# Kernel tuning notes

Hardware: AMD Instinct MI355X
Metric: run time of the kernel (lower is better)

## Reference

```python
import jax, jax.numpy as jnp
import numpy as np

NPOINT = 1024
NSAMPLE = 32
RADIUS = 0.2


def index_points2(points, idx):
    # points: (B,N,D), idx: (B,S) -> (B,S,D)
    return jnp.take_along_axis(points, idx[..., None], axis=1)


def index_points3(points, idx):
    # points: (B,N,D), idx: (B,S,K) -> (B,S,K,D)
    B, S, K = idx.shape
    flat = jnp.take_along_axis(points, idx.reshape(B, S * K)[..., None], axis=1)
    return flat.reshape(B, S, K, points.shape[-1])


def farthest_point_sampling(xyz, npoint):
    # xyz: (B,N,3) -> (B,npoint) int32 indices. First point deterministic (index 0).
    B, N, _ = xyz.shape
    first = jnp.zeros((B,), jnp.int32)
    chosen = jnp.zeros((B, npoint), jnp.int32).at[:, 0].set(first)
    first_xyz = index_points2(xyz, first[:, None])[:, 0, :]
    dist_min = jnp.sum((xyz - first_xyz[:, None, :]) ** 2, axis=-1)  # (B,N)

    def body(i, carry):
        chosen, dist_min = carry
        far = jnp.argmax(dist_min, axis=-1).astype(jnp.int32)  # (B,)
        far_xyz = index_points2(xyz, far[:, None])[:, 0, :]
        d = jnp.sum((xyz - far_xyz[:, None, :]) ** 2, axis=-1)
        return chosen.at[:, i].set(far), jnp.minimum(dist_min, d)

    chosen, _ = jax.lax.fori_loop(1, npoint, body, (chosen, dist_min))
    return chosen


def query_ball_point(radius, nsample, xyz, new_xyz):
    # (B,S,N) squared distances; out-of-ball -> inf; take nsample nearest (stable argsort).
    dist = jnp.sum((new_xyz[:, :, None, :] - xyz[:, None, :, :]) ** 2, axis=-1)
    dist_m = jnp.where(dist <= radius ** 2, dist, jnp.inf)
    return jnp.argsort(dist_m, axis=-1)[:, :, :nsample]


def mlp2(x, Wa, ba, Wb, bb, act2):
    h = jax.nn.relu(x @ Wa + ba)
    return act2(h @ Wb + bb)


def reference(xyz, features, W1, b1, W2, b2, W3, b3, W4, b4):
    fps_idx = farthest_point_sampling(xyz, NPOINT)          # (B,S)
    new_xyz = index_points2(xyz, fps_idx)                   # (B,S,3)
    group_idx = query_ball_point(RADIUS, NSAMPLE, xyz, new_xyz)  # (B,S,K)
    grouped_xyz = index_points3(xyz, group_idx)             # (B,S,K,3)
    grouped_xyz_norm = grouped_xyz - new_xyz[:, :, None, :]
    grouped_feats = index_points3(features, group_idx)      # (B,S,K,C)
    f_in = jnp.concatenate([grouped_xyz_norm, grouped_feats], axis=-1)
    f_prime = mlp2(f_in, W1, b1, W2, b2, jax.nn.relu)       # (B,S,K,H)
    f_mean = jnp.mean(f_prime, axis=2, keepdims=True)
    w_in = jnp.concatenate([grouped_xyz_norm, f_prime - f_mean], axis=-1)
    alpha = mlp2(w_in, W3, b3, W4, b4, jax.nn.sigmoid)      # (B,S,K,H)
    f_out = jnp.sum(alpha * f_prime, axis=2)                # (B,S,H)
    return new_xyz, f_out


def setup_inputs() -> dict:
    key = jax.random.key(0)
    ks = jax.random.split(key, 8)
    B, N, C, H = 16, 4096, 64, 128
    xyz = jax.random.uniform(ks[0], (B, N, 3), dtype=jnp.float32)
    features = jax.random.normal(ks[1], (B, N, C), dtype=jnp.float32)
    s = 0.1
    return {
        "xyz": xyz,
        "features": features,
        "W1": jax.random.normal(ks[2], (3 + C, H), dtype=jnp.float32) * s,
        "b1": jnp.zeros((H,), jnp.float32),
        "W2": jax.random.normal(ks[3], (H, H), dtype=jnp.float32) * s,
        "b2": jnp.zeros((H,), jnp.float32),
        "W3": jax.random.normal(ks[4], (3 + H, H), dtype=jnp.float32) * s,
        "b3": jnp.zeros((H,), jnp.float32),
        "W4": jax.random.normal(ks[5], (H, H), dtype=jnp.float32) * s,
        "b4": jnp.zeros((H,), jnp.float32),
    }
```

## Files before the change

kernel.cpp:

```cpp
#include <hip/hip_runtime.h>

typedef unsigned short u16;
typedef unsigned int   u32;
typedef unsigned long long u64;
typedef short s8v __attribute__((ext_vector_type(8)));
typedef float f4v __attribute__((ext_vector_type(4)));
typedef float f2v __attribute__((ext_vector_type(2)));
typedef unsigned long long ull2 __attribute__((ext_vector_type(2)));

#define STRIDE 168
#define CAP 256
#define OFF_G1 0
#define OFF_G2 12288
#define OFF_G3 28672
#define OFF_G4 49152
#define NBLK 240
#define PAIR_TASKS 2048

__device__ u32 g_prog[16*16];
__device__ u32 g_ticket[8*16];

__device__ __forceinline__ u16 f2bf(float f){
  u32 u = __float_as_uint(f);
  return (u16)((u + 0x7FFFu + ((u>>16)&1u)) >> 16);
}
__device__ __forceinline__ float sqd(float ax,float ay,float az,float bx,float by,float bz){
  float dx=ax-bx, dy=ay-by, dz=az-bz;
  return __fadd_rn(__fadd_rn(__fmul_rn(dx,dx),__fmul_rn(dy,dy)),__fmul_rn(dz,dz));
}

#define WMAX_STEP(v, CTRL) { \
  u32 _t = (u32)__builtin_amdgcn_update_dpp(0, (int)(v), CTRL, 0xf, 0xf, false); \
  (v) = (v) > _t ? (v) : _t; }
#define QMAX64(k, CTRL) { \
  u32 _lo=(u32)(k), _hi=(u32)((k)>>32); \
  u32 _plo=(u32)__builtin_amdgcn_update_dpp(0,(int)_lo,CTRL,0xf,0xf,true); \
  u32 _phi=(u32)__builtin_amdgcn_update_dpp(0,(int)_hi,CTRL,0xf,0xf,true); \
  u64 _o=((u64)_phi<<32)|_plo; (k) = (k)>_o ? (k) : _o; }

__device__ __forceinline__ void st_rlx(u32* p, u32 v){
  __hip_atomic_store(p, v, __ATOMIC_RELAXED, __HIP_MEMORY_SCOPE_AGENT);
}
__device__ __forceinline__ u32 ld_rlx(const u32* p){
  return __hip_atomic_load(p, __ATOMIC_RELAXED, __HIP_MEMORY_SCOPE_AGENT);
}

__global__ __launch_bounds__(256) void swz_kernel(const float* __restrict__ W1,const float* __restrict__ W2,
                                                  const float* __restrict__ W3,const float* __restrict__ W4,
                                                  u16* __restrict__ wsw){
  int T = blockIdx.x*256 + threadIdx.x;
  const float* W; int rel, base, kind;
  if(T < 1536){ rel=T;      base=OFF_G1; W=W1; kind=0; }
  else if(T < 3584){ rel=T-1536; base=OFF_G2; W=W2; kind=1; }
  else if(T < 6144){ rel=T-3584; base=OFF_G3; W=W3; kind=0; }
  else         { rel=T-6144; base=OFF_G4; W=W4; kind=1; }
  int chunk=rel>>6, lane=rel&63, c=chunk>>3, t=chunk&7, quad=lane>>4, l15=lane&15;
  u16 v[8];
  #pragma unroll
  for(int j=0;j<8;j++){
    int kp = c*32 + quad*8 + j, n = t*16 + l15;
    int src = (kind==0) ? (kp<3 ? kp : (kp>=32 ? kp-29 : -1)) : kp;
    v[j] = (src<0) ? (u16)0 : f2bf(W[src*128 + n]);
  }
  int4 o;
  o.x=(int)((u32)v[0]|((u32)v[1]<<16)); o.y=(int)((u32)v[2]|((u32)v[3]<<16));
  o.z=(int)((u32)v[4]|((u32)v[5]<<16)); o.w=(int)((u32)v[6]|((u32)v[7]<<16));
  *(int4*)&wsw[base + rel*8] = o;
  if(T==0){
    #pragma unroll
    for(int i=0;i<256;i++) g_prog[i]=0;
    #pragma unroll
    for(int i=0;i<128;i++) g_ticket[i]=0;
  }
}

__device__ __forceinline__ void zero_C(f4v C[2][8]){
  #pragma unroll
  for(int mt=0;mt<2;mt++)
    #pragma unroll
    for(int t=0;t<8;t++) C[mt][t] = (f4v){0.f,0.f,0.f,0.f};
}
__device__ __forceinline__ void load_bias(const float* bsrc,int l15,float bb[8]){
  #pragma unroll
  for(int t=0;t<8;t++) bb[t]=bsrc[t*16+l15];
}
template<int KC>
__device__ __forceinline__ void run_gemm(const u16* A, const u16* BW,
                                         int lane,int l15,int quad, f4v C[2][8]){
  s8v af[2][KC];
  #pragma unroll
  for(int mt=0;mt<2;mt++)
    #pragma unroll
    for(int c=0;c<KC;c++)
      af[mt][c] = *(const s8v*)&A[(mt*16+l15)*STRIDE + c*32 + quad*8];
  #pragma unroll
  for(int t=0;t<8;t++){
    #pragma unroll
    for(int c=0;c<KC;c++){
      s8v bw = *(const s8v*)&BW[((c*8+t)*64 + lane)*8];
      C[0][t] = __builtin_amdgcn_mfma_f32_16x16x32_bf16(af[0][c],bw,C[0][t],0,0,0);
      C[1][t] = __builtin_amdgcn_mfma_f32_16x16x32_bf16(af[1][c],bw,C[1][t],0,0,0);
    }
  }
}
__device__ __forceinline__ void store_act(u16* A,int l15,int quad,f4v C[2][8],const float bb[8]){
  #pragma unroll
  for(int mt=0;mt<2;mt++)
    #pragma unroll
    for(int t=0;t<8;t++)
      #pragma unroll
      for(int r=0;r<4;r++){
        float v = fmaxf(C[mt][t][r]+bb[t], 0.f);
        A[(mt*16+quad*4+r)*STRIDE + t*16 + l15] = f2bf(v);
      }
}
__device__ __forceinline__ void write_xyz_chunk0(u16* A,int lane,float xn,float yn,float zn){
  if(lane<32){
    u16* row=&A[lane*STRIDE];
    row[0]=f2bf(xn); row[1]=f2bf(yn); row[2]=f2bf(zn); row[3]=0;
    #pragma unroll
    for(int q=0;q<7;q++) *(u64*)&row[4+q*4] = 0ull;
  }
}

union SMem {
  struct { float S[4096*3]; u64 red[2][8]; } f;
  struct { u64 Bc[8][CAP+2]; int sel[8][32]; u16 A[8][32*STRIDE]; } c;
};

__global__ __launch_bounds__(512,2) void fused_kernel(const float* __restrict__ xyz,
    const float* __restrict__ feats, const u16* __restrict__ wsw,
    const float* __restrict__ b1,const float* __restrict__ b2,
    const float* __restrict__ b3,const float* __restrict__ b4,
    float* __restrict__ newxyz, float* __restrict__ fout){
  __shared__ __align__(16) SMem U;
  const int tid=threadIdx.x, lane=tid&63, wv=tid>>6;

  if(blockIdx.x < 16){
    const int b = blockIdx.x;
    float* S = U.f.S;
    const float* xb = xyz + (size_t)b*4096*3;
    #pragma unroll
    for(int j=0;j<6;j++) ((float4*)S)[j*512+tid] = ((const float4*)xb)[j*512+tid];
    __syncthreads();
    f2v X[4],Y[4],Z[4],DM[4];
    const float x0=S[0], y0=S[1], z0=S[2];
    {
      #pragma clang fp contract(off)
      const f2v fx2={x0,x0}, fy2={y0,y0}, fz2={z0,z0};
      #pragma unroll
      for(int k2=0;k2<4;k2++){
        int p0 = tid*8 + 2*k2;
        X[k2] = (f2v){S[p0*3],   S[p0*3+3]};
        Y[k2] = (f2v){S[p0*3+1], S[p0*3+4]};
        Z[k2] = (f2v){S[p0*3+2], S[p0*3+5]};
        f2v dx=X[k2]-fx2, dy=Y[k2]-fy2, dz=Z[k2]-fz2;
        DM[k2] = (dx*dx + dy*dy) + dz*dz;
      }
    }
    u32* nbu = (u32*)(newxyz + (size_t)b*3072);
    if(tid==0){
      st_rlx(&nbu[0], __float_as_uint(x0));
      st_rlx(&nbu[1], __float_as_uint(y0));
      st_rlx(&nbu[2], __float_as_uint(z0));
    }
    for(int i=1;i<1024;i++){
      f2v a = __builtin_elementwise_max(DM[0],DM[1]);
      f2v cc = __builtin_elementwise_max(DM[2],DM[3]);
      f2v mm = __builtin_elementwise_max(a,cc);
      float vm = fmaxf(mm[0], mm[1]);
      u32 m8 = 0;
      #pragma unroll
      for(int j=0;j<8;j++) m8 |= (DM[j>>1][j&1]==vm) ? (1u<<j) : 0u;
      int jm = __ffs(m8)-1;
      u32 w = __float_as_uint(vm);
      WMAX_STEP(w, 0x111); WMAX_STEP(w, 0x112); WMAX_STEP(w, 0x114);
      WMAX_STEP(w, 0x118); WMAX_STEP(w, 0x142); WMAX_STEP(w, 0x143);
      u32 wm = (u32)__builtin_amdgcn_readlane((int)w, 63);
      u64 msk = __ballot(__float_as_uint(vm) == wm);
      int ldr = __ffsll((unsigned long long)msk) - 1;
      int pj  = __builtin_amdgcn_readlane(jm, ldr);
      int p   = (wv*64 + ldr)*8 + pj;
      if(lane==0) U.f.red[i&1][wv] = ((u64)wm<<32) | (u32)(~(u32)p);
      __syncthreads();
      u64 k = U.f.red[i&1][lane&7];
      QMAX64(k, 0x121); QMAX64(k, 0x122); QMAX64(k, 0x124);
      int far = (int)(~(u32)k) & 4095;
      float fx=S[far*3], fy=S[far*3+1], fz=S[far*3+2];
      if(tid==0){
        u32* r = nbu + (size_t)i*3;
        st_rlx(&r[0], __float_as_uint(fx));
        st_rlx(&r[1], __float_as_uint(fy));
        st_rlx(&r[2], __float_as_uint(fz));
        if((i&31)==31){
          __asm__ __volatile__("s_waitcnt vmcnt(3)" ::: "memory");
          st_rlx(&g_prog[b*16], (u32)i);
        }
      }
      {
        #pragma clang fp contract(off)
        const f2v fx2={fx,fx}, fy2={fy,fy}, fz2={fz,fz};
        #pragma unroll
        for(int k2c=0;k2c<4;k2c++){
          f2v dx=X[k2c]-fx2, dy=Y[k2c]-fy2, dz=Z[k2c]-fz2;
          f2v s2 = (dx*dx + dy*dy) + dz*dz;
          DM[k2c] = __builtin_elementwise_min(DM[k2c], s2);
        }
      }
    }
    if(tid==0){
      __asm__ __volatile__("s_waitcnt vmcnt(0)" ::: "memory");
      st_rlx(&g_prog[b*16], 1024u);
    }
  }
  __syncthreads();

  const int quad=lane>>4, l15=lane&15;
  u64* Bc   = U.c.Bc[wv];
  int* selw = U.c.sel[wv];
  u16* A    = U.c.A[wv];
  const u64 lt = (1ull<<lane)-1ull;
  u32 xcc;
  __asm__ __volatile__("s_getreg_b32 %0, hwreg(HW_REG_XCC_ID)" : "=s"(xcc));
  const int mypair = (int)(xcc & 7u);
  for(int pk=0; pk<8; pk++){
    const int pair = (mypair + pk) & 7;
    for(;;){
      int t;
      if(lane==0) t = (int)atomicAdd(&g_ticket[pair*16], 1u);
      t = __shfl(t, 0);
      if(t >= PAIR_TASKS) break;
      const int s = t>>1, tb = pair*2 + (t&1), widx = (tb<<10) + s;
      for(;;){
        u32 pr = ld_rlx(&g_prog[tb*16]);
        if(pr > (u32)s) break;
        __builtin_amdgcn_s_sleep(16);
      }
      __asm__ __volatile__("" ::: "memory");
      const float* xb = xyz + (size_t)tb*4096*3;
      const u32* cpu = (const u32*)(newxyz + (size_t)widx*3);
      const float cx = __uint_as_float(ld_rlx(&cpu[0]));
      const float cy = __uint_as_float(ld_rlx(&cpu[1]));
      const float cz = __uint_as_float(ld_rlx(&cpu[2]));

      int base=0;
      for(int kk=0;kk<64;kk++){
        int p = kk*64 + lane;
        float d = sqd(cx,cy,cz, xb[p*3],xb[p*3+1],xb[p*3+2]);
        bool in = (d <= 0.04f);
        u64 m = __ballot(in);
        if(in){ int pos = base + __popcll(m&lt); if(pos<CAP) Bc[pos] = ((u64)__float_as_uint(d)<<32)|(u32)p; }
        base += __popcll(m);
      }
      int cnt = base>CAP ? CAP : base;
      if(cnt > 32){
        if(lane==0){ Bc[cnt]=~0ull; Bc[cnt+1]=~0ull; }
        int cnt2 = (cnt+1)&~1;
        for(int c=lane; c<cnt; c+=64){
          u64 key = Bc[c]; int r=0;
          for(int t2=0;t2<cnt2;t2+=2){
            ull2 k2 = *(const ull2*)&Bc[t2];
            r += (k2[0] < key) ? 1 : 0;
            r += (k2[1] < key) ? 1 : 0;
          }
          if(r < 32) selw[r] = (int)(u32)key;
        }
      } else {
        for(int c=lane; c<cnt; c+=64) selw[c] = (int)(u32)Bc[c];
        int need = 32 - cnt, bq = 0;
        for(int kk=0; kk<64 && bq<need; kk++){
          int p = kk*64 + lane;
          float d = sqd(cx,cy,cz, xb[p*3],xb[p*3+1],xb[p*3+2]);
          bool o = !(d <= 0.04f);
          u64 m = __ballot(o);
          if(o){ int pos = bq + __popcll(m&lt); if(pos<need) selw[cnt+pos] = p; }
          bq += __popcll(m);
        }
      }

      const int gi_f = selw[lane>>1] & 4095;
      const int gi_x = selw[lane & 31] & 4095;
      {
        int r2=lane>>1, h=lane&1;
        const float* fs = feats + ((size_t)tb*4096 + gi_f)*64 + h*32;
        u16* fd = &A[r2*STRIDE + 32 + h*32];
        #pragma unroll
        for(int j=0;j<8;j++){
          float4 v4 = ((const float4*)fs)[j];
          u64 pk4 = (u64)f2bf(v4.x) | ((u64)f2bf(v4.y)<<16)
                  | ((u64)f2bf(v4.z)<<32) | ((u64)f2bf(v4.w)<<48);
          *(u64*)&fd[j*4] = pk4;
        }
      }
      float xn=0.f,yn=0.f,zn=0.f;
      if(lane<32){
        const float* xp = xb + (size_t)gi_x*3;
        xn = xp[0]-cx; yn = xp[1]-cy; zn = xp[2]-cz;
      }
      write_xyz_chunk0(A,lane,xn,yn,zn);

      f4v C[2][8]; float bb[8];
      zero_C(C); load_bias(b1,l15,bb);
      run_gemm<3>(A, wsw+OFF_G1, lane,l15,quad, C);
      store_act(A,l15,quad,C,bb);
      zero_C(C); load_bias(b2,l15,bb);
      run_gemm<4>(A, wsw+OFF_G2, lane,l15,quad, C);
      float fp[2][8][4]; float mean[8];
      #pragma unroll
      for(int t2=0;t2<8;t2++){
        float sm=0.f;
        #pragma unroll
        for(int mt=0;mt<2;mt++)
          #pragma unroll
          for(int r=0;r<4;r++){
            float v = fmaxf(C[mt][t2][r]+bb[t2], 0.f);
            fp[mt][t2][r]=v; sm+=v;
          }
        sm += __shfl_xor(sm,16); sm += __shfl_xor(sm,32);
        mean[t2] = sm*0.03125f;
      }
      #pragma unroll
      for(int mt=0;mt<2;mt++)
        #pragma unroll
        for(int t2=0;t2<8;t2++)
          #pragma unroll
          for(int r=0;r<4;r++)
            A[(mt*16+quad*4+r)*STRIDE + 32 + t2*16 + l15] = f2bf(fp[mt][t2][r]-mean[t2]);
      write_xyz_chunk0(A,lane,xn,yn,zn);
      zero_C(C); load_bias(b3,l15,bb);
      run_gemm<5>(A, wsw+OFF_G3, lane,l15,quad, C);
      store_act(A,l15,quad,C,bb);
      zero_C(C); load_bias(b4,l15,bb);
      run_gemm<4>(A, wsw+OFF_G4, lane,l15,quad, C);
      float* fo = fout + (size_t)widx*128;
      #pragma unroll
      for(int t2=0;t2<8;t2++){
        float part=0.f;
        #pragma unroll
        for(int mt=0;mt<2;mt++)
          #pragma unroll
          for(int r=0;r<4;r++){
            float pre = C[mt][t2][r]+bb[t2];
            float aa = 1.f/(1.f+__expf(-pre));
            part += aa*fp[mt][t2][r];
          }
        part += __shfl_xor(part,16); part += __shfl_xor(part,32);
        if(quad==0) fo[t2*16+l15] = part;
      }
    }
  }
}

extern "C" void kernel_launch(void* const* d_in, const int* in_sizes, int n_in,
                              void* d_out, int out_size, void* d_ws, size_t ws_size,
                              hipStream_t stream){
  (void)in_sizes; (void)n_in; (void)out_size; (void)ws_size;
  const float* xyz   = (const float*)d_in[0];
  const float* feats = (const float*)d_in[1];
  const float* W1 = (const float*)d_in[2]; const float* b1 = (const float*)d_in[3];
  const float* W2 = (const float*)d_in[4]; const float* b2 = (const float*)d_in[5];
  const float* W3 = (const float*)d_in[6]; const float* b3 = (const float*)d_in[7];
  const float* W4 = (const float*)d_in[8]; const float* b4 = (const float*)d_in[9];
  float* out = (float*)d_out;
  float* newxyz = out;
  float* fout   = out + 16*1024*3;
  u16* wsw = (u16*)d_ws;

  hipLaunchKernelGGL(swz_kernel, dim3(32), dim3(256), 0, stream, W1,W2,W3,W4, wsw);
  void* args[9];
  args[0]=(void*)&xyz;  args[1]=(void*)&feats; args[2]=(void*)&wsw;
  args[3]=(void*)&b1;   args[4]=(void*)&b2;    args[5]=(void*)&b3; args[6]=(void*)&b4;
  args[7]=(void*)&newxyz; args[8]=(void*)&fout;
  hipLaunchCooperativeKernel((void*)fused_kernel, dim3(NBLK), dim3(512), args, 0, stream);
}
```

Measured before the change: 827.7 us.

## Run FPS on four waves with barrier-free tagged LDS reduction

The farthest-point-sampling loop now runs on 4 of the 8 waves, each holding 16 points per lane. The per-iteration __syncthreads is replaced by spin-polling on tagged 64-bit LDS slots, so waves exchange their argmax candidates without a block-wide barrier. The other 4 waves sleep until a done flag is set. The LDS layout becomes a flat per-wave region instead of a union. The goal is lower per-iteration sync latency on the serial FPS critical path, at the cost of more registers per lane and spin-wait traffic on LDS.

```diff
diff --git a/kernel.cpp b/kernel.cpp
--- a/kernel.cpp
+++ b/kernel.cpp
@@ -16,6 +16,8 @@
 #define OFF_G4 49152
 #define NBLK 240
 #define PAIR_TASKS 2048
+#define WREG 12944
+#define HDR 160
 
 __device__ u32 g_prog[16*16];
 __device__ u32 g_ticket[8*16];
@@ -43,6 +45,12 @@
 }
 __device__ __forceinline__ u32 ld_rlx(const u32* p){
   return __hip_atomic_load(p, __ATOMIC_RELAXED, __HIP_MEMORY_SCOPE_AGENT);
+}
+__device__ __forceinline__ void st_lds64(u64* p, u64 v){
+  __hip_atomic_store(p, v, __ATOMIC_RELAXED, __HIP_MEMORY_SCOPE_WORKGROUP);
+}
+__device__ __forceinline__ u64 ld_lds64(const u64* p){
+  return __hip_atomic_load(p, __ATOMIC_RELAXED, __HIP_MEMORY_SCOPE_WORKGROUP);
 }
 
 __global__ __launch_bounds__(256) void swz_kernel(const float* __restrict__ W1,const float* __restrict__ W2,
@@ -123,102 +131,127 @@
   }
 }
 
-union SMem {
-  struct { float S[4096*3]; u64 red[2][8]; } f;
-  struct { u64 Bc[8][CAP+2]; int sel[8][32]; u16 A[8][32*STRIDE]; } c;
-};
-
 __global__ __launch_bounds__(512,2) void fused_kernel(const float* __restrict__ xyz,
     const float* __restrict__ feats, const u16* __restrict__ wsw,
     const float* __restrict__ b1,const float* __restrict__ b2,
     const float* __restrict__ b3,const float* __restrict__ b4,
     float* __restrict__ newxyz, float* __restrict__ fout){
-  __shared__ __align__(16) SMem U;
+  __shared__ __align__(16) char LB[HDR + 8*WREG];
   const int tid=threadIdx.x, lane=tid&63, wv=tid>>6;
+  u32* fps_done = (u32*)LB;
+  u64* red2 = (u64*)(LB + 16);
 
   if(blockIdx.x < 16){
     const int b = blockIdx.x;
-    float* S = U.f.S;
+    float* S = (float*)(LB + HDR);
     const float* xb = xyz + (size_t)b*4096*3;
     #pragma unroll
     for(int j=0;j<6;j++) ((float4*)S)[j*512+tid] = ((const float4*)xb)[j*512+tid];
+    if(tid==0){
+      *fps_done = 0;
+      #pragma unroll
+      for(int q=0;q<8;q++) red2[q] = ~0ull;
+    }
     __syncthreads();
-    f2v X[4],Y[4],Z[4],DM[4];
-    const float x0=S[0], y0=S[1], z0=S[2];
-    {
-      #pragma clang fp contract(off)
-      const f2v fx2={x0,x0}, fy2={y0,y0}, fz2={z0,z0};
-      #pragma unroll
-      for(int k2=0;k2<4;k2++){
-        int p0 = tid*8 + 2*k2;
-        X[k2] = (f2v){S[p0*3],   S[p0*3+3]};
-        Y[k2] = (f2v){S[p0*3+1], S[p0*3+4]};
-        Z[k2] = (f2v){S[p0*3+2], S[p0*3+5]};
-        f2v dx=X[k2]-fx2, dy=Y[k2]-fy2, dz=Z[k2]-fz2;
-        DM[k2] = (dx*dx + dy*dy) + dz*dz;
-      }
-    }
-    u32* nbu = (u32*)(newxyz + (size_t)b*3072);
-    if(tid==0){
-      st_rlx(&nbu[0], __float_as_uint(x0));
-      st_rlx(&nbu[1], __float_as_uint(y0));
-      st_rlx(&nbu[2], __float_as_uint(z0));
-    }
-    for(int i=1;i<1024;i++){
-      f2v a = __builtin_elementwise_max(DM[0],DM[1]);
-      f2v cc = __builtin_elementwise_max(DM[2],DM[3]);
-      f2v mm = __builtin_elementwise_max(a,cc);
-      float vm = fmaxf(mm[0], mm[1]);
-      u32 m8 = 0;
-      #pragma unroll
-      for(int j=0;j<8;j++) m8 |= (DM[j>>1][j&1]==vm) ? (1u<<j) : 0u;
-      int jm = __ffs(m8)-1;
-      u32 w = __float_as_uint(vm);
-      WMAX_STEP(w, 0x111); WMAX_STEP(w, 0x112); WMAX_STEP(w, 0x114);
-      WMAX_STEP(w, 0x118); WMAX_STEP(w, 0x142); WMAX_STEP(w, 0x143);
-      u32 wm = (u32)__builtin_amdgcn_readlane((int)w, 63);
-      u64 msk = __ballot(__float_as_uint(vm) == wm);
-      int ldr = __ffsll((unsigned long long)msk) - 1;
-      int pj  = __builtin_amdgcn_readlane(jm, ldr);
-      int p   = (wv*64 + ldr)*8 + pj;
-      if(lane==0) U.f.red[i&1][wv] = ((u64)wm<<32) | (u32)(~(u32)p);
-      __syncthreads();
-      u64 k = U.f.red[i&1][lane&7];
-      QMAX64(k, 0x121); QMAX64(k, 0x122); QMAX64(k, 0x124);
-      int far = (int)(~(u32)k) & 4095;
-      float fx=S[far*3], fy=S[far*3+1], fz=S[far*3+2];
-      if(tid==0){
-        u32* r = nbu + (size_t)i*3;
-        st_rlx(&r[0], __float_as_uint(fx));
-        st_rlx(&r[1], __float_as_uint(fy));
-        st_rlx(&r[2], __float_as_uint(fz));
-        if((i&31)==31){
-          __asm__ __volatile__("s_waitcnt vmcnt(3)" ::: "memory");
-          st_rlx(&g_prog[b*16], (u32)i);
-        }
-      }
+
+    if(wv < 4){
+      f2v X[8],Y[8],Z[8],DM[8];
+      const float x0=S[0], y0=S[1], z0=S[2];
       {
         #pragma clang fp contract(off)
-        const f2v fx2={fx,fx}, fy2={fy,fy}, fz2={fz,fz};
-        #pragma unroll
-        for(int k2c=0;k2c<4;k2c++){
-          f2v dx=X[k2c]-fx2, dy=Y[k2c]-fy2, dz=Z[k2c]-fz2;
-          f2v s2 = (dx*dx + dy*dy) + dz*dz;
-          DM[k2c] = __builtin_elementwise_min(DM[k2c], s2);
-        }
-      }
+        const f2v fx2={x0,x0}, fy2={y0,y0}, fz2={z0,z0};
+        #pragma unroll
+        for(int k2=0;k2<8;k2++){
+          int p0 = tid*16 + 2*k2;
+          X[k2] = (f2v){S[p0*3],   S[p0*3+3]};
+          Y[k2] = (f2v){S[p0*3+1], S[p0*3+4]};
+          Z[k2] = (f2v){S[p0*3+2], S[p0*3+5]};
+          f2v dx=X[k2]-fx2, dy=Y[k2]-fy2, dz=Z[k2]-fz2;
+          DM[k2] = (dx*dx + dy*dy) + dz*dz;
+        }
+      }
+      u32* nbu = (u32*)(newxyz + (size_t)b*3072);
+      if(tid==0){
+        st_rlx(&nbu[0], __float_as_uint(x0));
+        st_rlx(&nbu[1], __float_as_uint(y0));
+        st_rlx(&nbu[2], __float_as_uint(z0));
+      }
+      for(int i=1;i<1024;i++){
+        f2v a0 = __builtin_elementwise_max(DM[0],DM[1]);
+        f2v a1 = __builtin_elementwise_max(DM[2],DM[3]);
+        f2v a2 = __builtin_elementwise_max(DM[4],DM[5]);
+        f2v a3 = __builtin_elementwise_max(DM[6],DM[7]);
+        f2v b0 = __builtin_elementwise_max(a0,a1);
+        f2v b1v= __builtin_elementwise_max(a2,a3);
+        f2v mm = __builtin_elementwise_max(b0,b1v);
+        float vm = fmaxf(mm[0], mm[1]);
+        u32 m16 = 0;
+        #pragma unroll
+        for(int j=0;j<16;j++) m16 |= (DM[j>>1][j&1]==vm) ? (1u<<j) : 0u;
+        int jm = __ffs(m16)-1;
+        u32 w = __float_as_uint(vm);
+        WMAX_STEP(w, 0x111); WMAX_STEP(w, 0x112); WMAX_STEP(w, 0x114);
+        WMAX_STEP(w, 0x118); WMAX_STEP(w, 0x142); WMAX_STEP(w, 0x143);
+        u32 wm = (u32)__builtin_amdgcn_readlane((int)w, 63);
+        u64 msk = __ballot(__float_as_uint(vm) == wm);
+        int ldr = __ffsll((unsigned long long)msk) - 1;
+        int pj  = __builtin_amdgcn_readlane(jm, ldr);
+        int p   = (wv*64 + ldr)*16 + pj;
+        const u32 tag = (u32)i & 1023u;
+        u64 mykey = ((u64)wm<<32) | ((u64)(((u32)~p)&0xFFFu)<<20) | tag;
+        if(lane==0) st_lds64(&red2[(i&1)*4 + wv], mykey);
+        __asm__ __volatile__("" ::: "memory");
+        u64 k;
+        do { k = ld_lds64(&red2[(i&1)*4 + (lane&3)]); }
+        while(!__all((u32)(k & 1023ull) == tag));
+        QMAX64(k, 0xB1);
+        QMAX64(k, 0x4E);
+        int far = (int)((~(u32)(k>>20)) & 0xFFFu);
+        float fx=S[far*3], fy=S[far*3+1], fz=S[far*3+2];
+        if(tid==0){
+          u32* r = nbu + (size_t)i*3;
+          st_rlx(&r[0], __float_as_uint(fx));
+          st_rlx(&r[1], __float_as_uint(fy));
+          st_rlx(&r[2], __float_as_uint(fz));
+          if((i&31)==31){
+            __asm__ __volatile__("s_waitcnt vmcnt(3)" ::: "memory");
+            st_rlx(&g_prog[b*16], (u32)i);
+          }
+        }
+        {
+          #pragma clang fp contract(off)
+          const f2v fx2={fx,fx}, fy2={fy,fy}, fz2={fz,fz};
+          #pragma unroll
+          for(int k2c=0;k2c<8;k2c++){
+            f2v dx=X[k2c]-fx2, dy=Y[k2c]-fy2, dz=Z[k2c]-fz2;
+            f2v s2 = (dx*dx + dy*dy) + dz*dz;
+            DM[k2c] = __builtin_elementwise_min(DM[k2c], s2);
+          }
+        }
+      }
+      {
+        if(lane==0) st_lds64(&red2[0*4 + wv], 0ull);
+        __asm__ __volatile__("" ::: "memory");
+        u64 k;
+        do { k = ld_lds64(&red2[0*4 + (lane&3)]); }
+        while(!__all((u32)(k & 1023ull) == 0u));
+      }
+      if(tid==0){
+        __asm__ __volatile__("s_waitcnt vmcnt(0)" ::: "memory");
+        st_rlx(&g_prog[b*16], 1024u);
+        __hip_atomic_store(fps_done, 1u, __ATOMIC_RELAXED, __HIP_MEMORY_SCOPE_WORKGROUP);
+      }
+    } else {
+      while(__hip_atomic_load(fps_done, __ATOMIC_RELAXED, __HIP_MEMORY_SCOPE_WORKGROUP) == 0u)
+        __builtin_amdgcn_s_sleep(32);
     }
-    if(tid==0){
-      __asm__ __volatile__("s_waitcnt vmcnt(0)" ::: "memory");
-      st_rlx(&g_prog[b*16], 1024u);
-    }
-  }
-  __syncthreads();
+  }
 
   const int quad=lane>>4, l15=lane&15;
-  u64* Bc   = U.c.Bc[wv];
-  int* selw = U.c.sel[wv];
-  u16* A    = U.c.A[wv];
+  char* wr  = LB + HDR + wv*WREG;
+  u64* Bc   = (u64*)wr;
+  int* selw = (int*)(wr + 2064);
+  u16* A    = (u16*)(wr + 2192);
   const u64 lt = (1ull<<lane)-1ull;
   u32 xcc;
   __asm__ __volatile__("s_getreg_b32 %0, hwreg(HW_REG_XCC_ID)" : "=s"(xcc));
```

New measurement: 828.0 us, median of 2. About the same (+0.0%).
